# Performance work log

Hardware: AMD Instinct MI355X
Metric: run time of the kernel (lower is better)

Reference implementation:

```python
import jax, jax.numpy as jnp
import numpy as np

NUM_HEADS = 8


def setup_inputs() -> dict:
    key = jax.random.key(0)
    ks = jax.random.split(key, 9)
    B, C, H, W = 2, 64, 48, 48
    Ck, Cv, Co = 64, 64, 64
    s = lambda fan_in: 1.0 / np.sqrt(fan_in)
    return {
        "x": jax.random.normal(ks[0], (B, C, H, W), jnp.float32),
        "Wq": jax.random.normal(ks[1], (Ck, C), jnp.float32) * s(C),
        "bq": jnp.zeros((Ck,), jnp.float32),
        "Wk": jax.random.normal(ks[2], (Ck, C), jnp.float32) * s(C),
        "bk": jnp.zeros((Ck,), jnp.float32),
        "Wv": jax.random.normal(ks[3], (Cv, C), jnp.float32) * s(C),
        "bv": jnp.zeros((Cv,), jnp.float32),
        "Wo": jax.random.normal(ks[4], (Co, Cv), jnp.float32) * s(Cv),
        "bo": jnp.zeros((Co,), jnp.float32),
    }


def _conv1x1(x, W, b):
    # 1x1 conv == channel matmul: [B,C,H,W] x [O,C] -> [B,O,H,W]
    return jnp.einsum("oc,bchw->bohw", W, x) + b[None, :, None, None]


def reference(x, Wq, bq, Wk, bk, Wv, bv, Wo, bo):
    B, _, H, W_ = x.shape
    nh = NUM_HEADS
    Ck, Cv = Wq.shape[0], Wv.shape[0]
    d = Ck // nh
    L = H * W_

    # NOTE: original torch code scales q in place via a view, so returned q is scaled.
    q = _conv1x1(x, Wq, bq) * (d ** -0.5)
    k = _conv1x1(x, Wk, bk)
    v = _conv1x1(x, Wv, bv)

    qs = q.reshape(B, nh, d, L)          # [B,h,d,Lq]
    ks = k.reshape(B, nh, d, L)          # [B,h,d,Lk]
    vs = v.reshape(B, nh, Cv // nh, L)   # [B,h,dv,Lk]

    logits = jnp.einsum("bhdq,bhdk->bhqk", qs, ks)   # [B,h,Lq,Lk]
    # softmax over the QUERY axis (dim=2), as in the original nn.Softmax(dim=2)
    weights = jax.nn.softmax(logits, axis=2)
    o = jnp.einsum("bhck,bhqk->bhcq", vs, weights)   # [B,h,dv,Lq]

    o = o.reshape(B, Cv, H, W_)
    out = _conv1x1(o, Wo, bo)
    return out, q
```

## Files before the change

### kernel.cpp

```cpp
#include <hip/hip_runtime.h>

#define LL   2304
#define CCH  64
#define NHD  8

static constexpr float QSCALE = 0.35355339059327373f;
static constexpr float LOG2E  = 1.4426950408889634f;

typedef _Float16 half2_t  __attribute__((ext_vector_type(2)));
typedef _Float16 half4_t  __attribute__((ext_vector_type(4)));
typedef _Float16 half8_t  __attribute__((ext_vector_type(8)));
typedef float    float16_t __attribute__((ext_vector_type(16)));

__device__ __forceinline__ half2_t pk_f16(float a, float b) {
    return __builtin_bit_cast(half2_t, __builtin_amdgcn_cvt_pkrtz(a, b));
}


__global__ __launch_bounds__(256) void k_qkv(
    const float* __restrict__ x,
    const float* __restrict__ Wq, const float* __restrict__ bq,
    const float* __restrict__ Wk, const float* __restrict__ bk,
    const float* __restrict__ Wv, const float* __restrict__ bv,
    float* __restrict__ qout,
    _Float16* __restrict__ Qt, _Float16* __restrict__ Kt, _Float16* __restrict__ Vt)
{
    __shared__ float xs[64][32];
    __shared__ float wsm[64][64];
    const int t   = threadIdx.x;
    const int l0  = blockIdx.x * 32;
    const int b   = blockIdx.y;
    const int mat = blockIdx.z;
    const float* W    = (mat == 0) ? Wq : (mat == 1 ? Wk : Wv);
    const float* bias = (mat == 0) ? bq : (mat == 1 ? bk : bv);
    const float* xb = x + (long)b * CCH * LL;

    #pragma unroll
    for (int p = 0; p < 2; ++p) {
        int flat = (p * 256 + t) * 4;
        int c = flat >> 5, l = flat & 31;
        *(float4*)&xs[c][l] = *(const float4*)&xb[(long)c * LL + l0 + l];
    }
    #pragma unroll
    for (int p = 0; p < 4; ++p) {
        int flat = (p * 256 + t) * 4;
        int c = flat >> 6, l = flat & 63;
        *(float4*)&wsm[c][l] = *(const float4*)&W[flat];
    }
    __syncthreads();

    const int l  = t & 31;
    const int cg = t >> 5;
    float acc[8];
    #pragma unroll
    for (int j = 0; j < 8; ++j) acc[j] = 0.f;
    for (int cp = 0; cp < 64; ++cp) {
        float xv = xs[cp][l];
        #pragma unroll
        for (int j = 0; j < 8; ++j) acc[j] = fmaf(wsm[cg * 8 + j][cp], xv, acc[j]);
    }
    long row = (long)(b * NHD + cg) * LL + l0 + l;
    if (mat == 0) {
        half8_t pq;
        #pragma unroll
        for (int j = 0; j < 8; ++j) {
            float qv = (acc[j] + bias[cg * 8 + j]) * QSCALE;
            qout[((long)b * CCH + cg * 8 + j) * LL + l0 + l] = qv;
            pq[j] = (_Float16)(qv * LOG2E);
        }
        *(half8_t*)(Qt + row * 8) = pq;
    } else if (mat == 1) {
        half8_t pk;
        #pragma unroll
        for (int j = 0; j < 8; ++j) pk[j] = (_Float16)(acc[j] + bias[cg * 8 + j]);
        *(half8_t*)(Kt + row * 8) = pk;
    } else {
        half8_t pv;
        #pragma unroll
        for (int j = 0; j < 8; ++j) pv[j] = (_Float16)(acc[j] + bias[cg * 8 + j]);
        *(half8_t*)(Vt + row * 8) = pv;
    }
}

__global__ __launch_bounds__(256) void k_denom(
    const _Float16* __restrict__ Qt, const _Float16* __restrict__ Kt,
    const _Float16* __restrict__ Vt, _Float16* __restrict__ V2)
{
    __shared__ _Float16 lQ[2][256][4];
    __shared__ float Dp[4][32];
    __shared__ float rDs[32];
    const int t    = threadIdx.x;
    const int bh   = blockIdx.y;
    const int k0   = blockIdx.x * 32;
    const int lane = t & 63, w = t >> 6;
    const int half = lane >> 5, l31 = lane & 31;

    half4_t kA = *(const half4_t*)(Kt + ((long)bh * LL + k0 + l31) * 8 + half * 4);

    const float4* qbase = (const float4*)(Qt + (long)bh * LL * 8);
    float4 pre = qbase[t];

    float16_t Dacc = {};
    for (int ch = 0; ch < 9; ++ch) {
        __syncthreads();
        *(float2*)&lQ[0][t][0] = make_float2(pre.x, pre.y);
        *(float2*)&lQ[1][t][0] = make_float2(pre.z, pre.w);
        __syncthreads();
        if (ch + 1 < 9) pre = qbase[(ch + 1) * 256 + t];
        #pragma unroll
        for (int T = 0; T < 2; ++T) {
            half4_t qB = *(const half4_t*)&lQ[half][(2 * w + T) * 32 + l31][0];
            float16_t S = __builtin_amdgcn_mfma_f32_32x32x8f16(kA, qB, (float16_t){}, 0, 0, 0);
            #pragma unroll
            for (int r = 0; r < 16; ++r) Dacc[r] += __builtin_amdgcn_exp2f(S[r]);
        }
    }
    #pragma unroll
    for (int r = 0; r < 16; ++r) {
        float v = Dacc[r];
        v += __shfl_xor(v, 1);  v += __shfl_xor(v, 2);  v += __shfl_xor(v, 4);
        v += __shfl_xor(v, 8);  v += __shfl_xor(v, 16);
        Dacc[r] = v;
    }
    if (l31 == 0) {
        #pragma unroll
        for (int r = 0; r < 16; ++r) {
            int row = (r & 3) + 8 * (r >> 2) + 4 * half;
            Dp[w][row] = Dacc[r];
        }
    }
    __syncthreads();
    if (t < 32) rDs[t] = 256.0f / (Dp[0][t] + Dp[1][t] + Dp[2][t] + Dp[3][t]);
    __syncthreads();
    {
        int kk = t >> 3, c = t & 7;
        float v = (float)Vt[((long)bh * LL + k0 + kk) * 8 + c];
        V2[((long)bh * 8 + c) * LL + k0 + kk] = (_Float16)(v * rDs[kk]);
    }
}

__global__ __launch_bounds__(256) void k_av(
    const _Float16* __restrict__ Qt, const _Float16* __restrict__ Kt,
    const _Float16* __restrict__ V2, float* __restrict__ ot)
{
    __shared__ _Float16 lK[2][64][4];
    __shared__ _Float16 lVt[8][72];
    const int t    = threadIdx.x;
    const int bh   = blockIdx.y;
    const int s    = blockIdx.z;
    const int b = bh >> 3, h = bh & 7;
    const int lane = t & 63, w = t >> 6;
    const int half = lane >> 5, l31 = lane & 31;
    const int q0   = blockIdx.x * 128 + w * 32;

    half4_t qB = *(const half4_t*)(Qt + ((long)bh * LL + q0 + l31) * 8 + half * 4);

    const long ks0 = (long)s * 576;
    const float4*    kbase = (const float4*)(Kt + ((long)bh * LL + ks0) * 8);
    const _Float16*  vbase = V2 + (long)bh * 8 * LL + ks0;

    float4 preK, preV;
    if (t < 64) preK = kbase[t];
    else if (t < 128) {
        int c = (t - 64) >> 3, j8 = (t - 64) & 7;
        preV = *(const float4*)(vbase + (long)c * LL + j8 * 8);
    }

    float16_t O = {};
    for (int ch = 0; ch < 9; ++ch) {
        __syncthreads();
        if (t < 64) {
            *(float2*)&lK[0][t][0] = make_float2(preK.x, preK.y);
            *(float2*)&lK[1][t][0] = make_float2(preK.z, preK.w);
        } else if (t < 128) {
            int c = (t - 64) >> 3, j8 = (t - 64) & 7;
            *(float4*)&lVt[c][j8 * 8] = preV;
        }
        __syncthreads();
        if (ch + 1 < 9) {
            if (t < 64) preK = kbase[(ch + 1) * 64 + t];
            else if (t < 128) {
                int c = (t - 64) >> 3, j8 = (t - 64) & 7;
                preV = *(const float4*)(vbase + (long)c * LL + (ch + 1) * 64 + j8 * 8);
            }
        }
        const int cl = l31 & 7;
        #pragma unroll
        for (int T = 0; T < 2; ++T) {
            int kb = T * 32;
            half4_t kA = *(const half4_t*)&lK[half][kb + l31][0];
            float16_t S = __builtin_amdgcn_mfma_f32_32x32x8f16(kA, qB, (float16_t){}, 0, 0, 0);
            #pragma unroll
            for (int g = 0; g < 4; ++g) {
                half2_t p0 = pk_f16(__builtin_amdgcn_exp2f(S[4 * g + 0]),
                                    __builtin_amdgcn_exp2f(S[4 * g + 1]));
                half2_t p1 = pk_f16(__builtin_amdgcn_exp2f(S[4 * g + 2]),
                                    __builtin_amdgcn_exp2f(S[4 * g + 3]));
                half4_t pB = __builtin_shufflevector(p0, p1, 0, 1, 2, 3);
                half4_t vA = *(const half4_t*)&lVt[cl][kb + g * 8 + half * 4];
                O = __builtin_amdgcn_mfma_f32_32x32x8f16(vA, pB, O, 0, 0, 0);
            }
        }
    }
    float* otb = ot + (long)s * (2 * CCH * LL) + ((long)b * CCH + h * 8) * LL;
    #pragma unroll
    for (int r = 0; r < 4; ++r) {
        int c = r + 4 * half;
        otb[(long)c * LL + q0 + l31] = O[r] * (1.0f / 256.0f);
    }
}

__global__ __launch_bounds__(256) void k_out(
    const float* __restrict__ ot, const float* __restrict__ Wo,
    const float* __restrict__ bo, float* __restrict__ out)
{
    __shared__ float os[64][32];
    __shared__ float wsm[64][64];
    const int t  = threadIdx.x;
    const int l0 = blockIdx.x * 32;
    const int b  = blockIdx.y;
    const long SLAB = 2 * CCH * (long)LL;
    const float* ob = ot + (long)b * CCH * LL;

    #pragma unroll
    for (int p = 0; p < 2; ++p) {
        int flat = (p * 256 + t) * 4;
        int cv = flat >> 5, l = flat & 31;
        long off = (long)cv * LL + l0 + l;
        float4 a = *(const float4*)&ob[off];
        #pragma unroll
        for (int s = 1; s < 4; ++s) {
            float4 bb = *(const float4*)&ob[s * SLAB + off];
            a.x += bb.x; a.y += bb.y; a.z += bb.z; a.w += bb.w;
        }
        *(float4*)&os[cv][l] = a;
    }
    #pragma unroll
    for (int p = 0; p < 4; ++p) {
        int flat = (p * 256 + t) * 4;
        int c = flat >> 6, l = flat & 63;
        *(float4*)&wsm[c][l] = *(const float4*)&Wo[flat];
    }
    __syncthreads();

    const int l  = t & 31;
    const int cg = t >> 5;
    float acc[8];
    #pragma unroll
    for (int j = 0; j < 8; ++j) acc[j] = 0.f;
    for (int cv = 0; cv < 64; ++cv) {
        float xv = os[cv][l];
        #pragma unroll
        for (int j = 0; j < 8; ++j) acc[j] = fmaf(wsm[cg * 8 + j][cv], xv, acc[j]);
    }
    #pragma unroll
    for (int j = 0; j < 8; ++j) {
        int co = cg * 8 + j;
        out[((long)b * CCH + co) * LL + l0 + l] = acc[j] + bo[co];
    }
}

extern "C" void kernel_launch(void* const* d_in, const int* in_sizes, int n_in,
                              void* d_out, int out_size, void* d_ws, size_t ws_size,
                              hipStream_t stream)
{
    const float* x  = (const float*)d_in[0];
    const float* Wq = (const float*)d_in[1];
    const float* bq = (const float*)d_in[2];
    const float* Wk = (const float*)d_in[3];
    const float* bk = (const float*)d_in[4];
    const float* Wv = (const float*)d_in[5];
    const float* bv = (const float*)d_in[6];
    const float* Wo = (const float*)d_in[7];
    const float* bo = (const float*)d_in[8];

    float* out  = (float*)d_out;
    float* qout = out + 294912;

    _Float16* Qt = (_Float16*)d_ws;
    _Float16* Kt = Qt + 294912;
    _Float16* Vt = Kt + 294912;
    _Float16* V2 = Vt + 294912;
    float*    ot = (float*)(V2 + 294912);

    k_qkv  <<<dim3(72, 2, 3),  256, 0, stream>>>(x, Wq, bq, Wk, bk, Wv, bv, qout, Qt, Kt, Vt);
    k_denom<<<dim3(72, 16),    256, 0, stream>>>(Qt, Kt, Vt, V2);
    k_av   <<<dim3(18, 16, 4), 256, 0, stream>>>(Qt, Kt, V2, ot);
    k_out  <<<dim3(72, 2),     256, 0, stream>>>(ot, Wo, bo, out);
}
```

Before: 110.2 us.

## Double-buffer LDS tiles in denom and AV kernels, split keys six ways

Both attention kernels now use double-buffered shared-memory tiles, so each loop iteration needs one barrier instead of two and the global prefetch overlaps the MFMA/exp work. The AV kernel splits keys into 6 chunks of 384 instead of 4 of 576, loads 128-key tiles with all 256 threads, and keeps two independent MFMA accumulators to break the dependency chain. The output kernel sums 6 partial slabs instead of 4. This costs more LDS per block and more partial-sum traffic through the workspace, which must be large enough for the extra slabs.

```diff
diff --git a/kernel.cpp b/kernel.cpp
--- a/kernel.cpp
+++ b/kernel.cpp
@@ -86,7 +86,7 @@
     const _Float16* __restrict__ Qt, const _Float16* __restrict__ Kt,
     const _Float16* __restrict__ Vt, _Float16* __restrict__ V2)
 {
-    __shared__ _Float16 lQ[2][256][4];
+    __shared__ _Float16 lQ[2][2][256][4];
     __shared__ float Dp[4][32];
     __shared__ float rDs[32];
     const int t    = threadIdx.x;
@@ -99,34 +99,46 @@
 
     const float4* qbase = (const float4*)(Qt + (long)bh * LL * 8);
     float4 pre = qbase[t];
-
-    float16_t Dacc = {};
+    *(float2*)&lQ[0][0][t][0] = make_float2(pre.x, pre.y);
+    *(float2*)&lQ[0][1][t][0] = make_float2(pre.z, pre.w);
+    __syncthreads();
+
+    float16_t D0 = {}, D1 = {};
     for (int ch = 0; ch < 9; ++ch) {
-        __syncthreads();
-        *(float2*)&lQ[0][t][0] = make_float2(pre.x, pre.y);
-        *(float2*)&lQ[1][t][0] = make_float2(pre.z, pre.w);
-        __syncthreads();
+        const int buf = ch & 1;
         if (ch + 1 < 9) pre = qbase[(ch + 1) * 256 + t];
-        #pragma unroll
-        for (int T = 0; T < 2; ++T) {
-            half4_t qB = *(const half4_t*)&lQ[half][(2 * w + T) * 32 + l31][0];
+        {
+            half4_t qB = *(const half4_t*)&lQ[buf][half][(2 * w + 0) * 32 + l31][0];
             float16_t S = __builtin_amdgcn_mfma_f32_32x32x8f16(kA, qB, (float16_t){}, 0, 0, 0);
             #pragma unroll
-            for (int r = 0; r < 16; ++r) Dacc[r] += __builtin_amdgcn_exp2f(S[r]);
+            for (int r = 0; r < 16; ++r) D0[r] += __builtin_amdgcn_exp2f(S[r]);
+        }
+        {
+            half4_t qB = *(const half4_t*)&lQ[buf][half][(2 * w + 1) * 32 + l31][0];
+            float16_t S = __builtin_amdgcn_mfma_f32_32x32x8f16(kA, qB, (float16_t){}, 0, 0, 0);
+            #pragma unroll
+            for (int r = 0; r < 16; ++r) D1[r] += __builtin_amdgcn_exp2f(S[r]);
+        }
+        if (ch + 1 < 9) {
+            const int nb = (ch + 1) & 1;
+            *(float2*)&lQ[nb][0][t][0] = make_float2(pre.x, pre.y);
+            *(float2*)&lQ[nb][1][t][0] = make_float2(pre.z, pre.w);
+            __syncthreads();
         }
     }
     #pragma unroll
     for (int r = 0; r < 16; ++r) {
-        float v = Dacc[r];
+        float v = D0[r] + D1[r];
         v += __shfl_xor(v, 1);  v += __shfl_xor(v, 2);  v += __shfl_xor(v, 4);
         v += __shfl_xor(v, 8);  v += __shfl_xor(v, 16);
-        Dacc[r] = v;
-    }
+        D0[r] = v;
+    }
+    __syncthreads();
     if (l31 == 0) {
         #pragma unroll
         for (int r = 0; r < 16; ++r) {
             int row = (r & 3) + 8 * (r >> 2) + 4 * half;
-            Dp[w][row] = Dacc[r];
+            Dp[w][row] = D0[r];
         }
     }
     __syncthreads();
@@ -143,8 +155,8 @@
     const _Float16* __restrict__ Qt, const _Float16* __restrict__ Kt,
     const _Float16* __restrict__ V2, float* __restrict__ ot)
 {
-    __shared__ _Float16 lK[2][64][4];
-    __shared__ _Float16 lVt[8][72];
+    __shared__ _Float16 lK[2][2][128][4];
+    __shared__ _Float16 lVt[2][8][136];
     const int t    = threadIdx.x;
     const int bh   = blockIdx.y;
     const int s    = blockIdx.z;
@@ -155,40 +167,35 @@
 
     half4_t qB = *(const half4_t*)(Qt + ((long)bh * LL + q0 + l31) * 8 + half * 4);
 
-    const long ks0 = (long)s * 576;
-    const float4*    kbase = (const float4*)(Kt + ((long)bh * LL + ks0) * 8);
-    const _Float16*  vbase = V2 + (long)bh * 8 * LL + ks0;
-
-    float4 preK, preV;
-    if (t < 64) preK = kbase[t];
-    else if (t < 128) {
-        int c = (t - 64) >> 3, j8 = (t - 64) & 7;
-        preV = *(const float4*)(vbase + (long)c * LL + j8 * 8);
-    }
-
-    float16_t O = {};
-    for (int ch = 0; ch < 9; ++ch) {
-        __syncthreads();
-        if (t < 64) {
-            *(float2*)&lK[0][t][0] = make_float2(preK.x, preK.y);
-            *(float2*)&lK[1][t][0] = make_float2(preK.z, preK.w);
-        } else if (t < 128) {
-            int c = (t - 64) >> 3, j8 = (t - 64) & 7;
-            *(float4*)&lVt[c][j8 * 8] = preV;
-        }
-        __syncthreads();
-        if (ch + 1 < 9) {
-            if (t < 64) preK = kbase[(ch + 1) * 64 + t];
-            else if (t < 128) {
-                int c = (t - 64) >> 3, j8 = (t - 64) & 7;
-                preV = *(const float4*)(vbase + (long)c * LL + (ch + 1) * 64 + j8 * 8);
-            }
-        }
-        const int cl = l31 & 7;
-        #pragma unroll
-        for (int T = 0; T < 2; ++T) {
+    const long ks0 = (long)s * 384;
+    const float4*   kbase = (const float4*)(Kt + ((long)bh * LL + ks0) * 8);
+    const _Float16* vbase = V2 + (long)bh * 8 * LL + ks0;
+
+    const int vc = (t - 128) >> 4, vj = (t - 128) & 15;
+    float4 pre;
+    if (t < 128) pre = kbase[t];
+    else         pre = *(const float4*)(vbase + (long)vc * LL + vj * 8);
+
+    if (t < 128) {
+        *(float2*)&lK[0][0][t][0] = make_float2(pre.x, pre.y);
+        *(float2*)&lK[0][1][t][0] = make_float2(pre.z, pre.w);
+    } else {
+        *(float4*)&lVt[0][vc][vj * 8] = pre;
+    }
+    __syncthreads();
+
+    float16_t O0 = {}, O1 = {};
+    const int cl = l31 & 7;
+    for (int ch = 0; ch < 3; ++ch) {
+        const int buf = ch & 1;
+        if (ch + 1 < 3) {
+            if (t < 128) pre = kbase[(ch + 1) * 128 + t];
+            else         pre = *(const float4*)(vbase + (long)vc * LL + (ch + 1) * 128 + vj * 8);
+        }
+        #pragma unroll
+        for (int T = 0; T < 4; ++T) {
             int kb = T * 32;
-            half4_t kA = *(const half4_t*)&lK[half][kb + l31][0];
+            half4_t kA = *(const half4_t*)&lK[buf][half][kb + l31][0];
             float16_t S = __builtin_amdgcn_mfma_f32_32x32x8f16(kA, qB, (float16_t){}, 0, 0, 0);
             #pragma unroll
             for (int g = 0; g < 4; ++g) {
@@ -197,16 +204,27 @@
                 half2_t p1 = pk_f16(__builtin_amdgcn_exp2f(S[4 * g + 2]),
                                     __builtin_amdgcn_exp2f(S[4 * g + 3]));
                 half4_t pB = __builtin_shufflevector(p0, p1, 0, 1, 2, 3);
-                half4_t vA = *(const half4_t*)&lVt[cl][kb + g * 8 + half * 4];
-                O = __builtin_amdgcn_mfma_f32_32x32x8f16(vA, pB, O, 0, 0, 0);
+                half4_t vA = *(const half4_t*)&lVt[buf][cl][kb + g * 8 + half * 4];
+                if (T & 1) O1 = __builtin_amdgcn_mfma_f32_32x32x8f16(vA, pB, O1, 0, 0, 0);
+                else       O0 = __builtin_amdgcn_mfma_f32_32x32x8f16(vA, pB, O0, 0, 0, 0);
             }
+        }
+        if (ch + 1 < 3) {
+            const int nb = (ch + 1) & 1;
+            if (t < 128) {
+                *(float2*)&lK[nb][0][t][0] = make_float2(pre.x, pre.y);
+                *(float2*)&lK[nb][1][t][0] = make_float2(pre.z, pre.w);
+            } else {
+                *(float4*)&lVt[nb][vc][vj * 8] = pre;
+            }
+            __syncthreads();
         }
     }
     float* otb = ot + (long)s * (2 * CCH * LL) + ((long)b * CCH + h * 8) * LL;
     #pragma unroll
     for (int r = 0; r < 4; ++r) {
         int c = r + 4 * half;
-        otb[(long)c * LL + q0 + l31] = O[r] * (1.0f / 256.0f);
+        otb[(long)c * LL + q0 + l31] = (O0[r] + O1[r]) * (1.0f / 256.0f);
     }
 }
 
@@ -229,7 +247,7 @@
         long off = (long)cv * LL + l0 + l;
         float4 a = *(const float4*)&ob[off];
         #pragma unroll
-        for (int s = 1; s < 4; ++s) {
+        for (int s = 1; s < 6; ++s) {
             float4 bb = *(const float4*)&ob[s * SLAB + off];
             a.x += bb.x; a.y += bb.y; a.z += bb.z; a.w += bb.w;
         }
@@ -285,6 +303,6 @@
 
     k_qkv  <<<dim3(72, 2, 3),  256, 0, stream>>>(x, Wq, bq, Wk, bk, Wv, bv, qout, Qt, Kt, Vt);
     k_denom<<<dim3(72, 16),    256, 0, stream>>>(Qt, Kt, Vt, V2);
-    k_av   <<<dim3(18, 16, 4), 256, 0, stream>>>(Qt, Kt, V2, ot);
+    k_av   <<<dim3(18, 16, 6), 256, 0, stream>>>(Qt, Kt, V2, ot);
     k_out  <<<dim3(72, 2),     256, 0, stream>>>(ot, Wo, bo, out);
 }
```

After: 113.0 us. +2.6%, slower.
